# Optimization experiments

Hardware: AMD Instinct MI355X
Metric: run time of the kernel (lower is better)

Reference implementation:

```python
import jax, jax.numpy as jnp
import numpy as np

SQRT2 = 1.4142135623730951
INV_SQRT_2PI = 0.3989422804014327

def Phi(x):
    # standard normal CDF
    return 0.5 * (1.0 + jax.lax.erf(x / SQRT2))

def phi(x):
    # standard normal pdf
    return INV_SQRT_2PI * jnp.exp(-0.5 * x * x)

def phip(x):
    # derivative of the standard normal pdf
    return -x * phi(x)


def setup_inputs() -> dict:
    key = jax.random.key(0)
    k1, k2, k3 = jax.random.split(key, 3)
    bs, n, c, d = 4, 256, 96, 2
    xin = jax.random.normal(k1, (bs, n, d), dtype=jnp.float32)
    meanin = jax.random.normal(k2, (bs, n, c), dtype=jnp.float32)
    # SPD spatial covariance: A A^T / n + 0.5 I (eigenvalues >> 1e-6)
    A = jax.random.normal(k3, (bs, n, n), dtype=jnp.float32)
    kin = A @ jnp.swapaxes(A, -1, -2) / n + 0.5 * jnp.eye(n, dtype=jnp.float32)
    return {"xin": xin, "meanin": meanin, "kin": kin}


def reference(xin, meanin, kin):
    bs, n, c = meanin.shape
    eye = jnp.eye(n, dtype=kin.dtype)
    kin = kin + eye * 1e-6
    kdiag = jnp.diagonal(kin, axis1=-2, axis2=-1)            # (bs,n)
    stdin = jnp.sqrt(jnp.clip(kdiag[..., None], 1e-8))       # (bs,n,1)
    z = meanin / stdin
    Phis = Phi(z)
    phis = phi(z)
    Eh = meanin * Phis + stdin * phis                        # (bs,n,c)

    # 2x2 matrix K12 per (i,j): [[k_ii, k_ij], [k_ji, k_jj]] -- kept as scalars
    m00 = kdiag[:, :, None]                                  # (bs,n,1) -> broadcast (bs,n,n)
    m11 = kdiag[:, None, :]
    m01 = kin
    m10 = jnp.swapaxes(kin, -1, -2)

    # matrix square root of 2x2 SPD: (M + sqrt(det) I) / sqrt(tr + 2 sqrt(det))
    det = m00 * m11 - m01 * m10
    tr = m00 + m11
    s = jnp.sqrt(jnp.clip(det, 1e-8))
    t = jnp.clip(jnp.sqrt(tr + 2.0 * s), 1e-8)
    s00 = (m00 + s) / t
    s01 = m01 / t
    s10 = m10 / t
    s11 = (m11 + s) / t

    # inverse of the 2x2 sqrt
    dS = jnp.clip(s00 * s11 - s01 * s10, 1e-8)
    i00 = s11 / dS
    i01 = -s01 / dS
    i10 = -s10 / dS
    i11 = s00 / dS

    mi = meanin[:, :, None, :]                               # (bs,n,1,c)
    mj = meanin[:, None, :, :]                               # (bs,1,n,c)

    u1 = i00[..., None] * mi + i01[..., None] * mj           # (bs,n,n,c)
    u2 = i10[..., None] * mi + i11[..., None] * mj
    Phi1 = Phi(u1)
    Phi2 = Phi(u2)
    p1 = phi(u1)
    p2 = phi(u2)

    Psi = Phi1 * Phi2
    psi1 = p1 * Phi2
    psi2 = Phi1 * p2

    EhhT_Psi = (mi * mj + kin[..., None]) * Psi
    EhhT_psi1 = (mj * s00[..., None] + mi * s10[..., None]) * psi1
    EhhT_psi2 = (mj * s01[..., None] + mi * s11[..., None]) * psi2

    SHPhiS11 = s00[..., None] * s01[..., None] * phip(u1) * Phi2
    SHPhiS12 = s01[..., None] * s01[..., None] * p1 * p2
    SHPhiS22 = s01[..., None] * s11[..., None] * Phi1 * phip(u2)
    SHPhiS = SHPhiS11 + 2.0 * SHPhiS12 + SHPhiS22

    EhhT = EhhT_Psi + (EhhT_psi1 + EhhT_psi2) + SHPhiS
    covar = (EhhT - Eh[:, :, None, :] * Eh[:, None, :, :]).mean(-1)   # (bs,n,n)

    dvals = jnp.clip(
        ((meanin ** 2 + stdin ** 2) * Phis + meanin * stdin * phis - Eh ** 2).mean(-1),
        1e-6,
    )                                                        # (bs,n)
    diag_covar = dvals[..., None] * eye                      # diag_embed
    full_covar = jnp.where(diag_covar > 1e-7, diag_covar, covar)
    return (xin, Eh, full_covar + eye * 1e-6)
```

## Files before the change

kernel.cpp:

```cpp
#include <hip/hip_runtime.h>
#include <math.h>

#define BSZ 4
#define NN  256
#define CC  96

#define XIN_OFF  0
#define EH_OFF   2048
#define COV_OFF  100352

#define INV_SQRT_2PI 0.3989422804014327f
#define EXP2C       -0.7213475204444817f
#define PHI_P   0.33267253f
#define PHI_C1  0.1740121f
#define PHI_C2 -0.0479399f
#define PHI_C3  0.3739278f

__device__ __forceinline__ float phi_from_exp_s(float u, float e) {
    float t  = __builtin_amdgcn_rcpf(__builtin_fmaf(PHI_P, fabsf(u), 1.0f));
    float hp = __builtin_fmaf(__builtin_fmaf(PHI_C3, t, PHI_C2), t, PHI_C1) * t * e;
    return 0.5f + __builtin_copysignf(0.5f - hp, u);
}

__global__ __launch_bounds__(128) void relu_cov_row(
    const float* __restrict__ xin, const float* __restrict__ meanin,
    const float* __restrict__ kin, float* __restrict__ out)
{
    const int row = blockIdx.x;
    const int b   = row >> 8;
    const int i   = row & (NN - 1);
    const int tid = threadIdx.x;

    const float kd   = kin[((size_t)b * NN + i) * NN + i] + 1e-6f;
    const float var  = fmaxf(kd, 1e-8f);
    const float stdv = __builtin_amdgcn_sqrtf(var);
    const float rstd = __builtin_amdgcn_rcpf(stdv);

    float dterm = 0.0f;
    if (tid < CC) {
        float m  = meanin[(size_t)row * CC + tid];
        float z  = m * rstd;
        float e  = __builtin_amdgcn_exp2f(z * z * EXP2C);
        float ph = INV_SQRT_2PI * e;
        float Ph = phi_from_exp_s(z, e);
        float Eh = m * Ph + stdv * ph;
        out[EH_OFF + (size_t)row * CC + tid] = Eh;
        dterm = (m * m + var) * Ph + m * stdv * ph - Eh * Eh;
    } else if (tid < CC + 2) {
        int dd = tid - CC;
        out[XIN_OFF + (size_t)row * 2 + dd] = xin[(size_t)row * 2 + dd];
    }

    float v = dterm;
    v += __shfl_down(v, 32, 64);
    v += __shfl_down(v, 16, 64);
    v += __shfl_down(v,  8, 64);
    v += __shfl_down(v,  4, 64);
    v += __shfl_down(v,  2, 64);
    v += __shfl_down(v,  1, 64);
    __shared__ float wsum[2];
    if ((tid & 63) == 0) wsum[tid >> 6] = v;
    __syncthreads();
    if (tid == 0) {
        float dval = fmaxf((wsum[0] + wsum[1]) * (1.0f / 96.0f), 1e-6f);
        out[COV_OFF + ((size_t)b * NN + i) * NN + i] = dval + 1e-6f;
    }
}

__global__ __launch_bounds__(256) void relu_cov_pair(
    const float* __restrict__ meanin, const float* __restrict__ kin,
    const float* __restrict__ Eh, float* __restrict__ out)
{
    const int blk = blockIdx.x;
    const int b   = blk >> 7;
    const int i2  = blk & 127;
    const int p   = threadIdx.x;

    const int rowA = i2;
    const int rowB = 255 - i2;

    __shared__ __align__(16) float smA[CC], sEA[CC], smB[CC], sEB[CC];
    {
        const float* mA = meanin + ((size_t)(b * NN + rowA)) * CC;
        const float* eA = Eh     + ((size_t)(b * NN + rowA)) * CC;
        const float* mB = meanin + ((size_t)(b * NN + rowB)) * CC;
        const float* eB = Eh     + ((size_t)(b * NN + rowB)) * CC;
        if      (p < 96)  smA[p]       = mA[p];
        else if (p < 192) sEA[p - 96]  = eA[p - 96];
        if      (p < 96)  smB[p]       = mB[p];
        else if (p < 192) sEB[p - 96]  = eB[p - 96];
    }
    __syncthreads();

    if (p >= 255) return;

    const int  nfirst   = 255 - i2;
    const bool firstSeg = p < nfirst;
    const int  i = firstSeg ? rowA : rowB;
    const int  j = firstSeg ? (i2 + 1 + p) : (p + 1);

    const float* kb  = kin + (size_t)b * NN * NN;
    const float  m00 = kb[i * (NN + 1)] + 1e-6f;
    const float  m11 = kb[j * (NN + 1)] + 1e-6f;
    const float  m01 = kb[i * NN + j];

    const float det = __builtin_fmaf(-m01, m01, m00 * m11);
    const float s   = __builtin_amdgcn_sqrtf(fmaxf(det, 1e-8f));
    const float t   = fmaxf(__builtin_amdgcn_sqrtf(m00 + m11 + 2.0f * s), 1e-8f);
    const float rt  = __builtin_amdgcn_rcpf(t);
    const float s00 = (m00 + s) * rt;
    const float s01 = m01 * rt;
    const float s11 = (m11 + s) * rt;
    const float dS  = fmaxf(__builtin_fmaf(-s01, s01, s00 * s11), 1e-8f);
    const float rdS = __builtin_amdgcn_rcpf(dS);
    const float i00 = s11 * rdS;
    const float i01 = -s01 * rdS;
    const float i11 = s00 * rdS;
    const float qd = -INV_SQRT_2PI * s01 * s01 * s01 * rdS;
    const float qj =  INV_SQRT_2PI * s00 * s00 * s11 * rdS;
    const float qi =  INV_SQRT_2PI * s00 * s11 * s11 * rdS;
    const float c2 = 2.0f * INV_SQRT_2PI * INV_SQRT_2PI * s01 * s01;

    const float4* mjp = (const float4*)(meanin + ((size_t)(b * NN + j)) * CC);
    const float4* Ejp = (const float4*)(Eh     + ((size_t)(b * NN + j)) * CC);
    const float4* mip = (const float4*)(firstSeg ? smA : smB);
    const float4* Eip = (const float4*)(firstSeg ? sEA : sEB);

    float acc0 = 0.0f, acc1 = 0.0f, acc2 = 0.0f, acc3 = 0.0f;

    auto elem = [&](float mi, float mjv, float Ei, float Ej, float& acc) {
        float u1 = __builtin_fmaf(i01, mjv, i00 * mi);
        float u2 = __builtin_fmaf(i11, mjv, i01 * mi);
        float e1 = __builtin_amdgcn_exp2f(u1 * u1 * EXP2C);
        float e2 = __builtin_amdgcn_exp2f(u2 * u2 * EXP2C);
        float d1 = __builtin_fmaf(PHI_P, fabsf(u1), 1.0f);
        float d2 = __builtin_fmaf(PHI_P, fabsf(u2), 1.0f);
        float rp = __builtin_amdgcn_rcpf(d1 * d2);
        float t1 = d2 * rp;
        float t2 = d1 * rp;
        float hp1 = __builtin_fmaf(__builtin_fmaf(PHI_C3, t1, PHI_C2), t1, PHI_C1) * t1 * e1;
        float hp2 = __builtin_fmaf(__builtin_fmaf(PHI_C3, t2, PHI_C2), t2, PHI_C1) * t2 * e2;
        float Phi1 = 0.5f + __builtin_copysignf(0.5f - hp1, u1);
        float Phi2 = 0.5f + __builtin_copysignf(0.5f - hp2, u2);
        float a  = __builtin_fmaf(mi, mjv, m01);
        float bb = __builtin_fmaf(qd, mi, qj * mjv);
        float cc = __builtin_fmaf(qi, mi, qd * mjv);
        acc = __builtin_fmaf(a,  Phi1 * Phi2, acc);
        acc = __builtin_fmaf(bb, e1 * Phi2,  acc);
        acc = __builtin_fmaf(cc, e2 * Phi1,  acc);
        acc = __builtin_fmaf(c2, e1 * e2,    acc);
        acc = __builtin_fmaf(-Ei, Ej,        acc);
    };

#pragma unroll 4
    for (int q = 0; q < 24; ++q) {
        float4 mj4 = mjp[q];
        float4 Ej4 = Ejp[q];
        float4 mi4 = mip[q];
        float4 Ei4 = Eip[q];
        elem(mi4.x, mj4.x, Ei4.x, Ej4.x, acc0);
        elem(mi4.y, mj4.y, Ei4.y, Ej4.y, acc1);
        elem(mi4.z, mj4.z, Ei4.z, Ej4.z, acc2);
        elem(mi4.w, mj4.w, Ei4.w, Ej4.w, acc3);
    }

    float v = ((acc0 + acc1) + (acc2 + acc3)) * (1.0f / 96.0f);
    out[COV_OFF + ((size_t)(b * NN + i)) * NN + j] = v;
    out[COV_OFF + ((size_t)(b * NN + j)) * NN + i] = v;
}

extern "C" void kernel_launch(void* const* d_in, const int* in_sizes, int n_in,
                              void* d_out, int out_size, void* d_ws, size_t ws_size,
                              hipStream_t stream) {
    const float* xin    = (const float*)d_in[0];
    const float* meanin = (const float*)d_in[1];
    const float* kin    = (const float*)d_in[2];
    float* out = (float*)d_out;

    relu_cov_row<<<BSZ * NN, 128, 0, stream>>>(xin, meanin, kin, out);
    relu_cov_pair<<<BSZ * 128, 256, 0, stream>>>(meanin, kin, out + EH_OFF, out);
}
```

Before: 87.16 us.

## Tile pair kernel into 16x16 triangular blocks with channel split and combine pass

Replaces the row-pair work split with 16x16 upper-triangular tiles per batch, staging the i and j rows of meanin and Eh in LDS so each row is reused across 16 pairs. Channels are split in two halves across blockIdx.y, which doubles the grid, and a third kernel sums the partials and writes both symmetric entries. It also refactors the per-element accumulation to use fewer FMAs. The cost is computing the diagonal tiles fully, including redundant lower-half pairs, plus a workspace round trip and an extra launch.

```diff
diff --git a/kernel.cpp b/kernel.cpp
--- a/kernel.cpp
+++ b/kernel.cpp
@@ -4,6 +4,9 @@
 #define BSZ 4
 #define NN  256
 #define CC  96
+#define TT  16
+#define NTILES 136
+#define LSTR 52
 
 #define XIN_OFF  0
 #define EH_OFF   2048
@@ -20,6 +23,17 @@
     float t  = __builtin_amdgcn_rcpf(__builtin_fmaf(PHI_P, fabsf(u), 1.0f));
     float hp = __builtin_fmaf(__builtin_fmaf(PHI_C3, t, PHI_C2), t, PHI_C1) * t * e;
     return 0.5f + __builtin_copysignf(0.5f - hp, u);
+}
+
+__device__ __forceinline__ int tri_offset(int k) {
+    return k * TT - (k * (k - 1)) / 2;
+}
+__device__ __forceinline__ void tri_decode(int t, int& ti, int& tj) {
+    float disc = 1089.0f - 8.0f * (float)t;
+    ti = (int)((33.0f - __builtin_amdgcn_sqrtf(disc)) * 0.5f);
+    while (tri_offset(ti + 1) <= t) ++ti;
+    while (tri_offset(ti) > t) --ti;
+    tj = ti + (t - tri_offset(ti));
 }
 
 __global__ __launch_bounds__(128) void relu_cov_row(
@@ -69,35 +83,44 @@
 
 __global__ __launch_bounds__(256) void relu_cov_pair(
     const float* __restrict__ meanin, const float* __restrict__ kin,
-    const float* __restrict__ Eh, float* __restrict__ out)
+    const float* __restrict__ Eh, float* __restrict__ partial)
 {
-    const int blk = blockIdx.x;
-    const int b   = blk >> 7;
-    const int i2  = blk & 127;
-    const int p   = threadIdx.x;
-
-    const int rowA = i2;
-    const int rowB = 255 - i2;
-
-    __shared__ __align__(16) float smA[CC], sEA[CC], smB[CC], sEB[CC];
+    const int bx = blockIdx.x;
+    const int b  = bx / NTILES;
+    const int t  = bx - b * NTILES;
+    const int ch = blockIdx.y;
+    const int p  = threadIdx.x;
+
+    int ti, tj;
+    tri_decode(t, ti, tj);
+
+    __shared__ __align__(16) float lds[4 * TT * LSTR];
+    float* const smi = lds;
+    float* const sEi = lds + TT * LSTR;
+    float* const smj = lds + 2 * TT * LSTR;
+    float* const sEj = lds + 3 * TT * LSTR;
+
     {
-        const float* mA = meanin + ((size_t)(b * NN + rowA)) * CC;
-        const float* eA = Eh     + ((size_t)(b * NN + rowA)) * CC;
-        const float* mB = meanin + ((size_t)(b * NN + rowB)) * CC;
-        const float* eB = Eh     + ((size_t)(b * NN + rowB)) * CC;
-        if      (p < 96)  smA[p]       = mA[p];
-        else if (p < 192) sEA[p - 96]  = eA[p - 96];
-        if      (p < 96)  smB[p]       = mB[p];
-        else if (p < 192) sEB[p - 96]  = eB[p - 96];
+        int k = p;
+#pragma unroll
+        for (int it = 0; it < 3; ++it, k += 256) {
+            int arr = k / 192;
+            int rem = k - arr * 192;
+            int r   = rem / 12;
+            int q   = rem - r * 12;
+            const float* src = (arr == 0 || arr == 2) ? meanin : Eh;
+            int row = ((arr < 2) ? ti : tj) * TT + r;
+            float4 v = *((const float4*)(src + ((size_t)(b * NN + row)) * CC + ch * 48) + q);
+            float* dst = lds + arr * (TT * LSTR) + r * LSTR + q * 4;
+            *(float4*)dst = v;
+        }
     }
     __syncthreads();
 
-    if (p >= 255) return;
-
-    const int  nfirst   = 255 - i2;
-    const bool firstSeg = p < nfirst;
-    const int  i = firstSeg ? rowA : rowB;
-    const int  j = firstSeg ? (i2 + 1 + p) : (p + 1);
+    const int i_loc = p >> 4;
+    const int j_loc = p & 15;
+    const int i = ti * TT + i_loc;
+    const int j = tj * TT + j_loc;
 
     const float* kb  = kin + (size_t)b * NN * NN;
     const float  m00 = kb[i * (NN + 1)] + 1e-6f;
@@ -106,8 +129,8 @@
 
     const float det = __builtin_fmaf(-m01, m01, m00 * m11);
     const float s   = __builtin_amdgcn_sqrtf(fmaxf(det, 1e-8f));
-    const float t   = fmaxf(__builtin_amdgcn_sqrtf(m00 + m11 + 2.0f * s), 1e-8f);
-    const float rt  = __builtin_amdgcn_rcpf(t);
+    const float tt  = fmaxf(__builtin_amdgcn_sqrtf(m00 + m11 + 2.0f * s), 1e-8f);
+    const float rt  = __builtin_amdgcn_rcpf(tt);
     const float s00 = (m00 + s) * rt;
     const float s01 = m01 * rt;
     const float s11 = (m11 + s) * rt;
@@ -121,10 +144,10 @@
     const float qi =  INV_SQRT_2PI * s00 * s11 * s11 * rdS;
     const float c2 = 2.0f * INV_SQRT_2PI * INV_SQRT_2PI * s01 * s01;
 
-    const float4* mjp = (const float4*)(meanin + ((size_t)(b * NN + j)) * CC);
-    const float4* Ejp = (const float4*)(Eh     + ((size_t)(b * NN + j)) * CC);
-    const float4* mip = (const float4*)(firstSeg ? smA : smB);
-    const float4* Eip = (const float4*)(firstSeg ? sEA : sEB);
+    const float* Lmi = smi + i_loc * LSTR;
+    const float* LEi = sEi + i_loc * LSTR;
+    const float* Lmj = smj + j_loc * LSTR;
+    const float* LEj = sEj + j_loc * LSTR;
 
     float acc0 = 0.0f, acc1 = 0.0f, acc2 = 0.0f, acc3 = 0.0f;
 
@@ -145,26 +168,45 @@
         float a  = __builtin_fmaf(mi, mjv, m01);
         float bb = __builtin_fmaf(qd, mi, qj * mjv);
         float cc = __builtin_fmaf(qi, mi, qd * mjv);
-        acc = __builtin_fmaf(a,  Phi1 * Phi2, acc);
-        acc = __builtin_fmaf(bb, e1 * Phi2,  acc);
-        acc = __builtin_fmaf(cc, e2 * Phi1,  acc);
-        acc = __builtin_fmaf(c2, e1 * e2,    acc);
-        acc = __builtin_fmaf(-Ei, Ej,        acc);
+        float ta = __builtin_fmaf(a,  Phi1, bb * e1);
+        float tb = __builtin_fmaf(cc, Phi1, c2 * e1);
+        acc = __builtin_fmaf(Phi2, ta, acc);
+        acc = __builtin_fmaf(e2,   tb, acc);
+        acc = __builtin_fmaf(-Ei,  Ej, acc);
     };
 
 #pragma unroll 4
-    for (int q = 0; q < 24; ++q) {
-        float4 mj4 = mjp[q];
-        float4 Ej4 = Ejp[q];
-        float4 mi4 = mip[q];
-        float4 Ei4 = Eip[q];
+    for (int q = 0; q < 12; ++q) {
+        float4 mi4 = *(const float4*)(Lmi + q * 4);
+        float4 mj4 = *(const float4*)(Lmj + q * 4);
+        float4 Ei4 = *(const float4*)(LEi + q * 4);
+        float4 Ej4 = *(const float4*)(LEj + q * 4);
         elem(mi4.x, mj4.x, Ei4.x, Ej4.x, acc0);
         elem(mi4.y, mj4.y, Ei4.y, Ej4.y, acc1);
         elem(mi4.z, mj4.z, Ei4.z, Ej4.z, acc2);
         elem(mi4.w, mj4.w, Ei4.w, Ej4.w, acc3);
     }
 
-    float v = ((acc0 + acc1) + (acc2 + acc3)) * (1.0f / 96.0f);
+    partial[((size_t)bx * 2 + ch) * 256 + p] = (acc0 + acc1) + (acc2 + acc3);
+}
+
+__global__ __launch_bounds__(256) void relu_cov_combine(
+    const float* __restrict__ partial, float* __restrict__ out)
+{
+    const int bx = blockIdx.x;
+    const int b  = bx / NTILES;
+    const int t  = bx - b * NTILES;
+    const int p  = threadIdx.x;
+
+    int ti, tj;
+    tri_decode(t, ti, tj);
+    const int i = ti * TT + (p >> 4);
+    const int j = tj * TT + (p & 15);
+    if (i >= j) return;
+
+    const float* base = partial + ((size_t)bx * 2) * 256 + p;
+    float v = (base[0] + base[256]) * (1.0f / 96.0f);
+
     out[COV_OFF + ((size_t)(b * NN + i)) * NN + j] = v;
     out[COV_OFF + ((size_t)(b * NN + j)) * NN + i] = v;
 }
@@ -175,8 +217,11 @@
     const float* xin    = (const float*)d_in[0];
     const float* meanin = (const float*)d_in[1];
     const float* kin    = (const float*)d_in[2];
-    float* out = (float*)d_out;
+    float* out     = (float*)d_out;
+    float* partial = (float*)d_ws;
 
     relu_cov_row<<<BSZ * NN, 128, 0, stream>>>(xin, meanin, kin, out);
-    relu_cov_pair<<<BSZ * 128, 256, 0, stream>>>(meanin, kin, out + EH_OFF, out);
-}
+    relu_cov_pair<<<dim3(BSZ * NTILES, 2), 256, 0, stream>>>(
+        meanin, kin, out + EH_OFF, partial);
+    relu_cov_combine<<<BSZ * NTILES, 256, 0, stream>>>(partial, out);
+}
```

Result: faster. 77.72 us (-10.8%).
